# Optimization experiments

Measured on AMD Instinct MI355X. Metric: run time of the kernel, lower is better.

Reference implementation:

```python
import jax, jax.numpy as jnp
import numpy as np

N_NODES = 100000
N_EDGES = 1200000
IN_DIM = 64
HID = 64
N_GRAPHS = 512
N_CLASSES = 1
LN_EPS = 1e-5
NORM_EPS = 1e-12


def _layer_norm(x, g, b):
    mu = x.mean(-1, keepdims=True)
    var = ((x - mu) ** 2).mean(-1, keepdims=True)
    return (x - mu) * jax.lax.rsqrt(var + LN_EPS) * g + b


def setup_inputs() -> dict:
    key = jax.random.key(0)
    ks = jax.random.split(key, 20)
    h = jax.random.normal(ks[0], (N_NODES, IN_DIM), jnp.float32)
    src = jax.random.randint(ks[1], (N_EDGES,), 0, N_NODES)
    dst = jax.random.randint(ks[2], (N_EDGES,), 0, N_NODES)
    graph_ids = jnp.sort(jax.random.randint(ks[3], (N_NODES,), 0, N_GRAPHS))
    s1 = 1.0 / np.sqrt(IN_DIM)
    s2 = 1.0 / np.sqrt(HID)
    s3 = 1.0 / np.sqrt(2 * HID)
    return {
        "h": h, "src": src, "dst": dst, "graph_ids": graph_ids,
        "W1": jax.random.normal(ks[4], (IN_DIM, HID), jnp.float32) * s1,
        "b1": jnp.zeros((HID,), jnp.float32),
        "W2": jax.random.normal(ks[5], (HID, HID), jnp.float32) * s2,
        "b2": jnp.zeros((HID,), jnp.float32),
        "g1": jnp.ones((HID,), jnp.float32), "be1": jnp.zeros((HID,), jnp.float32),
        "g2": jnp.ones((HID,), jnp.float32), "be2": jnp.zeros((HID,), jnp.float32),
        "g3": jnp.ones((HID,), jnp.float32), "be3": jnp.zeros((HID,), jnp.float32),
        "g4": jnp.ones((HID,), jnp.float32), "be4": jnp.zeros((HID,), jnp.float32),
        "Wc1": jax.random.normal(ks[6], (2 * HID, HID), jnp.float32) * s3,
        "bc1": jnp.zeros((HID,), jnp.float32),
        "Wc2": jax.random.normal(ks[7], (HID, HID), jnp.float32) * s2,
        "bc2": jnp.zeros((HID,), jnp.float32),
        "Wc3": jax.random.normal(ks[8], (HID, N_CLASSES), jnp.float32) * s2,
        "bc3": jnp.zeros((N_CLASSES,), jnp.float32),
    }


def reference(h, src, dst, graph_ids, W1, b1, W2, b2, g1, be1, g2, be2,
              g3, be3, g4, be4, Wc1, bc1, Wc2, bc2, Wc3, bc3):
    N = N_NODES
    ones_e = jnp.ones((src.shape[0],), jnp.float32)
    # DGL GraphConv norm='both': symmetric degree normalization (clamp 0 -> 1)
    deg_out = jnp.clip(jax.ops.segment_sum(ones_e, src, num_segments=N), 1.0)
    deg_in = jnp.clip(jax.ops.segment_sum(ones_e, dst, num_segments=N), 1.0)
    ns = (deg_out ** -0.5)[:, None]
    nd = (deg_in ** -0.5)[:, None]

    def conv(x, W, b):
        msg = (x * ns)[src]                                  # [E, d] gather
        agg = jax.ops.segment_sum(msg, dst, num_segments=N)  # [N, d] scatter-add
        return (agg * nd) @ W + b

    h1 = jax.nn.relu(_layer_norm(conv(h, W1, b1), g1, be1))
    h1 = jax.nn.relu(_layer_norm(conv(h1, W2, b2), g2, be2))

    # per-graph mean / max pooling (dgl.mean_nodes / dgl.max_nodes)
    ssum = jax.ops.segment_sum(h1, graph_ids, num_segments=N_GRAPHS)
    cnt = jnp.clip(jax.ops.segment_sum(jnp.ones((N,), jnp.float32), graph_ids,
                                       num_segments=N_GRAPHS), 1.0)
    hg = ssum / cnt[:, None]
    hg_max = jax.ops.segment_max(h1, graph_ids, num_segments=N_GRAPHS)

    def l2norm(x):  # F.normalize(p=2, dim=1)
        n = jnp.sqrt((x * x).sum(-1, keepdims=True))
        return x / jnp.maximum(n, NORM_EPS)

    hg = jnp.concatenate([l2norm(hg), l2norm(hg_max)], axis=1)  # [G, 2*HID]
    out = jax.nn.relu(_layer_norm(hg @ Wc1 + bc1, g3, be3))
    out = jax.nn.relu(_layer_norm(out @ Wc2 + bc2, g4, be4))
    return out @ Wc3 + bc3
```

## Files before the change

kernel.cpp:

```cpp
#include <hip/hip_runtime.h>
#include <math.h>

#define HID 64
#define LN_EPS 1e-5f
#define NORM_EPS 1e-12f
#define CHUNK 1024

__device__ __forceinline__ float wave_sum64(float v) {
#pragma unroll
    for (int o = 32; o > 0; o >>= 1) v += __shfl_xor(v, o, 64);
    return v;
}

__global__ __launch_bounds__(256) void count_kernel(const int* __restrict__ src,
                                                    const int* __restrict__ dst,
                                                    int* __restrict__ cnt_out,
                                                    int* __restrict__ cnt_in,
                                                    int E) {
    int e = blockIdx.x * 256 + threadIdx.x;
    if (e >= E) return;
    atomicAdd(&cnt_out[src[e]], 1);
    atomicAdd(&cnt_in[dst[e]], 1);
}

__global__ __launch_bounds__(256) void norm_kernel(int* __restrict__ cnt_out,
                                                   const int* __restrict__ cnt_in,
                                                   float* __restrict__ ns,
                                                   float* __restrict__ nd,
                                                   int N) {
    int n = blockIdx.x * 256 + threadIdx.x;
    if (n >= N) return;
    ns[n] = rsqrtf((float)max(cnt_out[n], 1));
    nd[n] = rsqrtf((float)max(cnt_in[n], 1));
    cnt_out[n] = 0;
}

__global__ __launch_bounds__(256) void scan1_kernel(const int* __restrict__ cnt,
                                                    int* __restrict__ cs,
                                                    int* __restrict__ partials,
                                                    int N) {
    __shared__ int wsum[4];
    int t = threadIdx.x;
    int lane = t & 63, wave = t >> 6;
    int base = blockIdx.x * CHUNK + t * 4;
    int v0 = (base + 0 < N) ? cnt[base + 0] : 0;
    int v1 = (base + 1 < N) ? cnt[base + 1] : 0;
    int v2 = (base + 2 < N) ? cnt[base + 2] : 0;
    int v3 = (base + 3 < N) ? cnt[base + 3] : 0;
    int tsum = v0 + v1 + v2 + v3;
    int x = tsum;
#pragma unroll
    for (int off = 1; off < 64; off <<= 1) {
        int y = __shfl_up(x, off, 64);
        if (lane >= off) x += y;
    }
    if (lane == 63) wsum[wave] = x;
    __syncthreads();
    int waveoff = 0;
    for (int w = 0; w < wave; ++w) waveoff += wsum[w];
    int off0 = waveoff + x - tsum;
    if (base + 0 < N) cs[base + 0] = off0;
    if (base + 1 < N) cs[base + 1] = off0 + v0;
    if (base + 2 < N) cs[base + 2] = off0 + v0 + v1;
    if (base + 3 < N) cs[base + 3] = off0 + v0 + v1 + v2;
    if (t == 255) partials[blockIdx.x] = waveoff + x;
}

__global__ __launch_bounds__(256) void scan2_kernel(int* __restrict__ partials, int nch) {
    __shared__ int wsum[4];
    int t = threadIdx.x;
    int lane = t & 63, wave = t >> 6;
    int base = t * 4;
    int v0 = (base + 0 < nch) ? partials[base + 0] : 0;
    int v1 = (base + 1 < nch) ? partials[base + 1] : 0;
    int v2 = (base + 2 < nch) ? partials[base + 2] : 0;
    int v3 = (base + 3 < nch) ? partials[base + 3] : 0;
    int tsum = v0 + v1 + v2 + v3;
    int x = tsum;
#pragma unroll
    for (int off = 1; off < 64; off <<= 1) {
        int y = __shfl_up(x, off, 64);
        if (lane >= off) x += y;
    }
    if (lane == 63) wsum[wave] = x;
    __syncthreads();
    int waveoff = 0;
    for (int w = 0; w < wave; ++w) waveoff += wsum[w];
    int off0 = waveoff + x - tsum;
    if (base + 0 < nch) partials[base + 0] = off0;
    if (base + 1 < nch) partials[base + 1] = off0 + v0;
    if (base + 2 < nch) partials[base + 2] = off0 + v0 + v1;
    if (base + 3 < nch) partials[base + 3] = off0 + v0 + v1 + v2;
}

__global__ __launch_bounds__(256) void scan3_kernel(int* __restrict__ cs,
                                                    const int* __restrict__ partials,
                                                    int N, int E) {
    int n = blockIdx.x * 256 + threadIdx.x;
    if (n < N) cs[n] += partials[n / CHUNK];
    if (n == 0) cs[N] = E;
}

__global__ __launch_bounds__(256) void fill_kernel(const int* __restrict__ src,
                                                   const int* __restrict__ dst,
                                                   const float* __restrict__ ns,
                                                   const int* __restrict__ cs,
                                                   int* __restrict__ cursor,
                                                   int2* __restrict__ epack,
                                                   int E) {
    int e = blockIdx.x * 256 + threadIdx.x;
    if (e >= E) return;
    int s = src[e];
    int d = dst[e];
    float w = ns[s];
    int p = cs[d] + atomicAdd(&cursor[d], 1);
    epack[p] = make_int2(s, __float_as_int(w));
}

__global__ __launch_bounds__(256) void conv_kernel(const float* __restrict__ x,
                                                   const int2* __restrict__ epack,
                                                   const int* __restrict__ cs,
                                                   const float* __restrict__ nd,
                                                   const float* __restrict__ W,
                                                   const float* __restrict__ b,
                                                   const float* __restrict__ gam,
                                                   const float* __restrict__ bet,
                                                   float* __restrict__ out,
                                                   int N) {
    __shared__ float Ws[HID * HID];
    __shared__ float ts[4][HID];
    int tid = threadIdx.x;
    for (int i = tid; i < HID * HID / 4; i += 256) {
        reinterpret_cast<float4*>(Ws)[i] = reinterpret_cast<const float4*>(W)[i];
    }
    int wave = tid >> 6;
    int lane = tid & 63;
    int n = blockIdx.x * 4 + wave;

    float acc = 0.0f;
    float t = 0.0f;
    if (n < N) {
        int beg = cs[n], end = cs[n + 1];
        for (int e = beg; e < end; ++e) {
            int2 p = epack[e];
            acc = fmaf(x[(size_t)p.x * HID + lane], __int_as_float(p.y), acc);
        }
        t = acc * nd[n];
    }
    __syncthreads();
    if (n >= N) return;
    ts[wave][lane] = t;

    float y = b[lane];
#pragma unroll 8
    for (int k = 0; k < HID; ++k) {
        y = fmaf(ts[wave][k], Ws[k * HID + lane], y);
    }
    float mu = wave_sum64(y) * (1.0f / HID);
    float d = y - mu;
    float var = wave_sum64(d * d) * (1.0f / HID);
    float o = d * rsqrtf(var + LN_EPS) * gam[lane] + bet[lane];
    o = fmaxf(o, 0.0f);
    out[(size_t)n * HID + lane] = o;
}

__global__ __launch_bounds__(256) void pool_kernel(const float* __restrict__ h1,
                                                   const int* __restrict__ gid,
                                                   float* __restrict__ gsum,
                                                   int* __restrict__ gmax,
                                                   float* __restrict__ gcnt,
                                                   int N) {
    int wave = threadIdx.x >> 6;
    int lane = threadIdx.x & 63;
    int strip = blockIdx.x * 4 + wave;
    int base = strip * 64;
    if (base >= N) return;
    int nmax = min(64, N - base);
    int gv = (base + lane < N) ? gid[base + lane] : -1;
    int gcur = __shfl(gv, 0, 64);
    float sum = 0.0f, mx = 0.0f;
    int cnt = 0;
    for (int i = 0; i < nmax; ++i) {
        int g = __shfl(gv, i, 64);
        if (g != gcur) {
            atomicAdd(&gsum[(size_t)gcur * HID + lane], sum);
            atomicMax(&gmax[(size_t)gcur * HID + lane], __float_as_int(mx));
            if (lane == 0) atomicAdd(&gcnt[gcur], (float)cnt);
            sum = 0.0f; mx = 0.0f; cnt = 0; gcur = g;
        }
        float v = h1[((size_t)base + i) * HID + lane];
        sum += v;
        mx = fmaxf(mx, v);
        cnt++;
    }
    atomicAdd(&gsum[(size_t)gcur * HID + lane], sum);
    atomicMax(&gmax[(size_t)gcur * HID + lane], __float_as_int(mx));
    if (lane == 0) atomicAdd(&gcnt[gcur], (float)cnt);
}

__global__ __launch_bounds__(64) void head_kernel(const float* __restrict__ gsum,
                                                  const int* __restrict__ gmax,
                                                  const float* __restrict__ gcnt,
                                                  const float* __restrict__ Wc1,
                                                  const float* __restrict__ bc1,
                                                  const float* __restrict__ g3,
                                                  const float* __restrict__ be3,
                                                  const float* __restrict__ Wc2,
                                                  const float* __restrict__ bc2,
                                                  const float* __restrict__ g4,
                                                  const float* __restrict__ be4,
                                                  const float* __restrict__ Wc3,
                                                  const float* __restrict__ bc3,
                                                  float* __restrict__ out) {
    __shared__ float hg[2 * HID];
    __shared__ float t1[HID];
    int g = blockIdx.x;
    int lane = threadIdx.x;

    float cnt = fmaxf(gcnt[g], 1.0f);
    float mean = gsum[(size_t)g * HID + lane] / cnt;
    float mx = __int_as_float(gmax[(size_t)g * HID + lane]);

    float s1 = sqrtf(wave_sum64(mean * mean));
    float a = mean / fmaxf(s1, NORM_EPS);
    float s2 = sqrtf(wave_sum64(mx * mx));
    float bmx = mx / fmaxf(s2, NORM_EPS);

    hg[lane] = a;
    hg[HID + lane] = bmx;
    __syncthreads();

    float y = bc1[lane];
#pragma unroll 8
    for (int k = 0; k < 2 * HID; ++k) {
        y = fmaf(hg[k], Wc1[k * HID + lane], y);
    }
    float mu = wave_sum64(y) * (1.0f / HID);
    float d = y - mu;
    float var = wave_sum64(d * d) * (1.0f / HID);
    float o = d * rsqrtf(var + LN_EPS) * g3[lane] + be3[lane];
    o = fmaxf(o, 0.0f);
    t1[lane] = o;
    __syncthreads();

    float y2 = bc2[lane];
#pragma unroll 8
    for (int k = 0; k < HID; ++k) {
        y2 = fmaf(t1[k], Wc2[k * HID + lane], y2);
    }
    mu = wave_sum64(y2) * (1.0f / HID);
    d = y2 - mu;
    var = wave_sum64(d * d) * (1.0f / HID);
    o = d * rsqrtf(var + LN_EPS) * g4[lane] + be4[lane];
    o = fmaxf(o, 0.0f);

    float v = o * Wc3[lane];
    v = wave_sum64(v);
    if (lane == 0) out[g] = v + bc3[0];
}

extern "C" void kernel_launch(void* const* d_in, const int* in_sizes, int n_in,
                              void* d_out, int out_size, void* d_ws, size_t ws_size,
                              hipStream_t stream) {
    const float* h   = (const float*)d_in[0];
    const int*   src = (const int*)d_in[1];
    const int*   dst = (const int*)d_in[2];
    const int*   gid = (const int*)d_in[3];
    const float* W1  = (const float*)d_in[4];
    const float* b1  = (const float*)d_in[5];
    const float* W2  = (const float*)d_in[6];
    const float* b2  = (const float*)d_in[7];
    const float* g1  = (const float*)d_in[8];
    const float* be1 = (const float*)d_in[9];
    const float* g2  = (const float*)d_in[10];
    const float* be2 = (const float*)d_in[11];
    const float* g3  = (const float*)d_in[12];
    const float* be3 = (const float*)d_in[13];
    const float* g4  = (const float*)d_in[14];
    const float* be4 = (const float*)d_in[15];
    const float* Wc1 = (const float*)d_in[16];
    const float* bc1 = (const float*)d_in[17];
    const float* Wc2 = (const float*)d_in[18];
    const float* bc2 = (const float*)d_in[19];
    const float* Wc3 = (const float*)d_in[20];
    const float* bc3 = (const float*)d_in[21];
    float* out = (float*)d_out;

    const int N = in_sizes[0] / HID;
    const int E = in_sizes[1];
    const int G = out_size;

    char* ws = (char*)d_ws;
    float* h1     = (float*)ws;
    float* h2     = h1 + (size_t)N * HID;
    int2*  epack  = (int2*)(h2 + (size_t)N * HID);
    float* ns     = (float*)(epack + E);
    float* nd     = ns + N;
    int*   cnt_out= (int*)(nd + N);
    int*   cnt_in = cnt_out + N;
    int*   cs     = cnt_in + N;
    int*   partials = cs + N + 4;
    float* gsum   = (float*)(partials + 1024);
    int*   gmax   = (int*)(gsum + (size_t)G * HID);
    float* gcnt   = (float*)(gmax + (size_t)G * HID);

    const int nch = (N + CHUNK - 1) / CHUNK;

    hipMemsetAsync(cnt_out, 0, sizeof(int) * (size_t)2 * N, stream);
    hipMemsetAsync(gsum, 0, sizeof(float) * (size_t)G * (2 * HID + 1), stream);

    count_kernel<<<(E + 255) / 256, 256, 0, stream>>>(src, dst, cnt_out, cnt_in, E);
    norm_kernel<<<(N + 255) / 256, 256, 0, stream>>>(cnt_out, cnt_in, ns, nd, N);
    scan1_kernel<<<nch, 256, 0, stream>>>(cnt_in, cs, partials, N);
    scan2_kernel<<<1, 256, 0, stream>>>(partials, nch);
    scan3_kernel<<<(N + 255) / 256, 256, 0, stream>>>(cs, partials, N, E);
    fill_kernel<<<(E + 255) / 256, 256, 0, stream>>>(src, dst, ns, cs, cnt_out, epack, E);

    conv_kernel<<<(N + 3) / 4, 256, 0, stream>>>(h, epack, cs, nd, W1, b1, g1, be1, h1, N);
    conv_kernel<<<(N + 3) / 4, 256, 0, stream>>>(h1, epack, cs, nd, W2, b2, g2, be2, h2, N);

    int nstrips = (N + 63) / 64;
    pool_kernel<<<(nstrips + 3) / 4, 256, 0, stream>>>(h2, gid, gsum, gmax, gcnt, N);

    head_kernel<<<G, 64, 0, stream>>>(gsum, gmax, gcnt, Wc1, bc1, g3, be3,
                                      Wc2, bc2, g4, be4, Wc3, bc3, out);
}
```

Baseline: 623.4 us.

## Make conv kernel persistent grid-stride, unroll gather, use shuffles for matvec

The conv kernel now launches a fixed grid of 2048 blocks that grid-stride over nodes, so the 16KB weight tile is loaded into shared memory once per block instead of once per 4 nodes. The edge gather loop is unrolled by 4 to keep more independent loads in flight, and the per-node 64x64 matvec broadcasts the aggregated vector with wave shuffles instead of a shared-memory staging array and a barrier. The cost is fewer blocks for hiding latency and a serial accumulation chain per lane, plus the shuffle overhead in the matvec.

```diff
diff --git a/kernel.cpp b/kernel.cpp
--- a/kernel.cpp
+++ b/kernel.cpp
@@ -5,6 +5,7 @@
 #define LN_EPS 1e-5f
 #define NORM_EPS 1e-12f
 #define CHUNK 1024
+#define CONV_BLOCKS 2048
 
 __device__ __forceinline__ float wave_sum64(float v) {
 #pragma unroll
@@ -128,40 +129,51 @@
                                                    float* __restrict__ out,
                                                    int N) {
     __shared__ float Ws[HID * HID];
-    __shared__ float ts[4][HID];
     int tid = threadIdx.x;
     for (int i = tid; i < HID * HID / 4; i += 256) {
         reinterpret_cast<float4*>(Ws)[i] = reinterpret_cast<const float4*>(W)[i];
     }
+    __syncthreads();
     int wave = tid >> 6;
     int lane = tid & 63;
-    int n = blockIdx.x * 4 + wave;
-
-    float acc = 0.0f;
-    float t = 0.0f;
-    if (n < N) {
+    float bl = b[lane], gl = gam[lane], bel = bet[lane];
+
+    for (int n = blockIdx.x * 4 + wave; n < N; n += CONV_BLOCKS * 4) {
         int beg = cs[n], end = cs[n + 1];
-        for (int e = beg; e < end; ++e) {
+        float acc = 0.0f;
+        int e = beg;
+        for (; e + 4 <= end; e += 4) {
+            int2 p0 = epack[e + 0];
+            int2 p1 = epack[e + 1];
+            int2 p2 = epack[e + 2];
+            int2 p3 = epack[e + 3];
+            float v0 = x[(size_t)p0.x * HID + lane];
+            float v1 = x[(size_t)p1.x * HID + lane];
+            float v2 = x[(size_t)p2.x * HID + lane];
+            float v3 = x[(size_t)p3.x * HID + lane];
+            acc = fmaf(v0, __int_as_float(p0.y), acc);
+            acc = fmaf(v1, __int_as_float(p1.y), acc);
+            acc = fmaf(v2, __int_as_float(p2.y), acc);
+            acc = fmaf(v3, __int_as_float(p3.y), acc);
+        }
+        for (; e < end; ++e) {
             int2 p = epack[e];
             acc = fmaf(x[(size_t)p.x * HID + lane], __int_as_float(p.y), acc);
         }
-        t = acc * nd[n];
-    }
-    __syncthreads();
-    if (n >= N) return;
-    ts[wave][lane] = t;
-
-    float y = b[lane];
-#pragma unroll 8
-    for (int k = 0; k < HID; ++k) {
-        y = fmaf(ts[wave][k], Ws[k * HID + lane], y);
-    }
-    float mu = wave_sum64(y) * (1.0f / HID);
-    float d = y - mu;
-    float var = wave_sum64(d * d) * (1.0f / HID);
-    float o = d * rsqrtf(var + LN_EPS) * gam[lane] + bet[lane];
-    o = fmaxf(o, 0.0f);
-    out[(size_t)n * HID + lane] = o;
+        float t = acc * nd[n];
+
+        float y = bl;
+#pragma unroll
+        for (int k = 0; k < HID; ++k) {
+            y = fmaf(__shfl(t, k, 64), Ws[k * HID + lane], y);
+        }
+        float mu = wave_sum64(y) * (1.0f / HID);
+        float d = y - mu;
+        float var = wave_sum64(d * d) * (1.0f / HID);
+        float o = d * rsqrtf(var + LN_EPS) * gl + bel;
+        o = fmaxf(o, 0.0f);
+        out[(size_t)n * HID + lane] = o;
+    }
 }
 
 __global__ __launch_bounds__(256) void pool_kernel(const float* __restrict__ h1,
@@ -316,8 +328,8 @@
     scan3_kernel<<<(N + 255) / 256, 256, 0, stream>>>(cs, partials, N, E);
     fill_kernel<<<(E + 255) / 256, 256, 0, stream>>>(src, dst, ns, cs, cnt_out, epack, E);
 
-    conv_kernel<<<(N + 3) / 4, 256, 0, stream>>>(h, epack, cs, nd, W1, b1, g1, be1, h1, N);
-    conv_kernel<<<(N + 3) / 4, 256, 0, stream>>>(h1, epack, cs, nd, W2, b2, g2, be2, h2, N);
+    conv_kernel<<<CONV_BLOCKS, 256, 0, stream>>>(h, epack, cs, nd, W1, b1, g1, be1, h1, N);
+    conv_kernel<<<CONV_BLOCKS, 256, 0, stream>>>(h1, epack, cs, nd, W2, b2, g2, be2, h2, N);
 
     int nstrips = (N + 63) / 64;
     pool_kernel<<<(nstrips + 3) / 4, 256, 0, stream>>>(h2, gid, gsum, gmax, gcnt, N);
```

New measurement: 539.4 us. -13.5%, faster.
